# Kernel tuning notes

Hardware: AMD Instinct MI355X
Metric: run time of the kernel (lower is better)

## Reference

```python
import jax, jax.numpy as jnp
import numpy as np

T, B, I, H, O = 512, 128, 512, 512, 12

def setup_inputs() -> dict:
    key = jax.random.key(0)
    ks = jax.random.split(key, 17)
    def w(k, shape):
        # xavier-normal-ish init
        std = float(np.sqrt(2.0 / (shape[0] + shape[-1])))
        return jax.random.normal(k, shape, dtype=jnp.float32) * std
    return {
        "x": jax.random.normal(ks[0], (T, B, I), dtype=jnp.float32),
        "w0": w(ks[1], (O, H)), "wz": w(ks[2], (O, H)), "wr": w(ks[3], (O, H)),
        "ws": w(ks[4], (I, H)),
        "wa": w(ks[5], (H, H)), "ua": w(ks[6], (I, H)), "va": w(ks[7], (H, 1)),
        "u0": w(ks[8], (H, H)), "uz": w(ks[9], (H, H)), "ur": w(ks[10], (H, H)),
        "c0": w(ks[11], (I, H)), "cz": w(ks[12], (I, H)), "cr": w(ks[13], (I, H)),
        "fc_w": w(ks[14], (H, O)),
        "fc_b": jnp.zeros((O,), dtype=jnp.float32),
        "max_labels": 16,
    }

def reference(x, w0, wz, wr, ws, wa, ua, va, u0, uz, ur, c0, cz, cr, fc_w, fc_b, max_labels):
    # x: [T, B, I] encoder states; decode max_labels steps of a Bahdanau-attention GRU.
    s0 = jnp.tanh(x[0] @ ws)              # [B, H]
    out0 = s0 @ fc_w + fc_b               # [B, O]
    U = jnp.einsum('tbi,ih->tbh', x, ua)  # precomputed encoder projection
    va_v = va[:, 0]                       # [H]

    def step(carry, _):
        s, out = carry                                          # [B,H], [B,O]
        e = jnp.einsum('tbh,h->tb', jnp.tanh(s @ wa + U), va_v)  # [T,B] additive scores
        a = jax.nn.softmax(e, axis=0)                           # attention over T
        c = jnp.einsum('tb,tbi->bi', a, x)                      # [B,I] context
        r = jax.nn.sigmoid(out @ wr + s @ ur + c @ cr)
        z = jax.nn.sigmoid(out @ wz + s @ uz + c @ cz)
        sh = jnp.tanh(out @ w0 + (r * s) @ u0 + c @ c0)
        s_new = (1.0 - z) * s + z * sh
        out_new = s_new @ fc_w + fc_b
        return (s_new, out_new), out_new

    _, outs = jax.lax.scan(step, (s0, out0), None, length=max_labels - 1)
    all_outs = jnp.concatenate([out0[None], outs], axis=0)  # [L, B, O]
    return jnp.transpose(all_outs, (1, 0, 2))               # [B, L, O]
```

## Files before the change

kernel.cpp:

```cpp
#include <hip/hip_runtime.h>

#define NSTEP 16

typedef __attribute__((ext_vector_type(8))) short s16x8;
typedef __attribute__((ext_vector_type(4))) float f32x4;
typedef __attribute__((ext_vector_type(2))) float f32x2;

__device__ __forceinline__ float bf2f(unsigned short u){
  union { unsigned int i; float f; } v; v.i = ((unsigned int)u) << 16; return v.f;
}
__device__ __forceinline__ unsigned short f2bf(float f){
  union { float f; unsigned int i; } v; v.f = f;
  unsigned int r = v.i + 0x7fffu + ((v.i >> 16) & 1u);
  return (unsigned short)(r >> 16);
}
__device__ __forceinline__ float fast_rcp(float x){ return __builtin_amdgcn_rcpf(x); }
__device__ __forceinline__ float fast_tanh(float x){
  float e = __expf(2.0f * x);
  return 1.0f - 2.0f * fast_rcp(e + 1.0f);
}
__device__ __forceinline__ float fast_sigmoid(float x){
  return fast_rcp(1.0f + __expf(-x));
}
__device__ __forceinline__ void gload16(const void* g, void* l){
  __builtin_amdgcn_global_load_lds((const __attribute__((address_space(1))) void*)g,
                                   (__attribute__((address_space(3))) void*)l, 16, 0, 0);
}
__device__ __forceinline__ float wave_sum(float v){
#pragma unroll
  for (int off = 32; off; off >>= 1) v += __shfl_xor(v, off, 64);
  return v;
}
__device__ __forceinline__ void fp8x8_dec(uint2 w, float* u){
  f32x2 d0 = __builtin_amdgcn_cvt_pk_f32_fp8(w.x, false);
  f32x2 d1 = __builtin_amdgcn_cvt_pk_f32_fp8(w.x, true);
  f32x2 d2 = __builtin_amdgcn_cvt_pk_f32_fp8(w.y, false);
  f32x2 d3 = __builtin_amdgcn_cvt_pk_f32_fp8(w.y, true);
  u[0] = d0[0]; u[1] = d0[1]; u[2] = d1[0]; u[3] = d1[1];
  u[4] = d2[0]; u[5] = d2[1]; u[6] = d3[0]; u[7] = d3[1];
}
__device__ __forceinline__ s16x8 f32x8_to_bf8(float4 a, float4 b){
  s16x8 t8;
  t8[0] = (short)f2bf(a.x); t8[1] = (short)f2bf(a.y);
  t8[2] = (short)f2bf(a.z); t8[3] = (short)f2bf(a.w);
  t8[4] = (short)f2bf(b.x); t8[5] = (short)f2bf(b.y);
  t8[6] = (short)f2bf(b.z); t8[7] = (short)f2bf(b.w);
  return t8;
}
__device__ __forceinline__ uint2 f32x8_to_fp8(float4 a, float4 b){
  unsigned int lo, hi;
  lo = __builtin_amdgcn_cvt_pk_fp8_f32(a.x, a.y, 0, false);
  lo = __builtin_amdgcn_cvt_pk_fp8_f32(a.z, a.w, lo, true);
  hi = __builtin_amdgcn_cvt_pk_fp8_f32(b.x, b.y, 0, false);
  hi = __builtin_amdgcn_cvt_pk_fp8_f32(b.z, b.w, hi, true);
  uint2 w; w.x = lo; w.y = hi;
  return w;
}
__device__ __forceinline__ unsigned char f2fp8(float f){
  return (unsigned char)(__builtin_amdgcn_cvt_pk_fp8_f32(f, f, 0, false) & 0xff);
}

__global__ __launch_bounds__(256) void castx_k(const float* __restrict__ x,
                                               unsigned char* __restrict__ x8){
  size_t idx = (size_t)blockIdx.x * 256 + threadIdx.x;
  const float* p = x + idx * 8;
  float4 a = *(const float4*)p, b = *(const float4*)(p + 4);
  *(uint2*)(x8 + idx * 8) = f32x8_to_fp8(a, b);
}

struct G8LDS { unsigned char A[128 * 64]; unsigned char B[128 * 64]; };

__global__ __launch_bounds__(512) void ugemm8_k(
    const unsigned char* __restrict__ x8, const unsigned char* __restrict__ Pua8,
    unsigned char* __restrict__ U8){
  __shared__ G8LDS lds;
  const int tid = threadIdx.x;
  const int lane = tid & 63, wid = tid >> 6;
  const int wr = wid >> 2, wc = wid & 3;
  const int mt = blockIdx.y, nt = blockIdx.x;
  f32x4 acc[4][2];
#pragma unroll
  for (int m = 0; m < 4; ++m)
#pragma unroll
    for (int n = 0; n < 2; ++n) acc[m][n] = (f32x4)0.0f;

  const int row = tid >> 2, j = tid & 3;
  const int sc16 = j ^ (row & 3);
  for (int kt = 0; kt < 512; kt += 64){
    __syncthreads();
    gload16(x8  + (size_t)(mt * 128 + row) * 512 + kt + sc16 * 16, &lds.A[tid * 16]);
    gload16(Pua8 + (size_t)(nt * 128 + row) * 512 + kt + sc16 * 16, &lds.B[tid * 16]);
    __syncthreads();
#pragma unroll
    for (int ks = 0; ks < 2; ++ks){
      int g = (lane >> 4) + ks * 4;
      long av[4], bv[2];
#pragma unroll
      for (int m = 0; m < 4; ++m){
        int r = wr * 64 + m * 16 + (lane & 15);
        av[m] = *(const long*)&lds.A[r * 64 + ((g ^ ((r & 3) << 1)) << 3)];
      }
#pragma unroll
      for (int n = 0; n < 2; ++n){
        int c = wc * 32 + n * 16 + (lane & 15);
        bv[n] = *(const long*)&lds.B[c * 64 + ((g ^ ((c & 3) << 1)) << 3)];
      }
#pragma unroll
      for (int m = 0; m < 4; ++m)
#pragma unroll
        for (int n = 0; n < 2; ++n)
          acc[m][n] = __builtin_amdgcn_mfma_f32_16x16x32_fp8_fp8(av[m], bv[n], acc[m][n], 0, 0, 0);
    }
  }
#pragma unroll
  for (int m = 0; m < 4; ++m)
#pragma unroll
    for (int n = 0; n < 2; ++n){
      int r_base = mt * 128 + wr * 64 + m * 16 + ((lane >> 4) << 2);
      int col = nt * 128 + wc * 32 + n * 16 + (lane & 15);
#pragma unroll
      for (int q = 0; q < 4; ++q)
        U8[(size_t)(r_base + q) * 512 + col] = f2fp8(acc[m][n][q] * 0.125f);
    }
}

struct FLDS { unsigned short A[64 * 256]; unsigned short B[64 * 256]; };

template<int EPI, bool AF32>
__device__ __forceinline__ void fgemm_body(int mt, int nt,
    const unsigned short* __restrict__ A, const float* __restrict__ Af,
    const unsigned short* __restrict__ Bt,
    unsigned short* __restrict__ ob0, float* __restrict__ o0,
    const float* __restrict__ e0, const float* __restrict__ e1,
    const float* __restrict__ e2, FLDS& lds){
  const int tid = threadIdx.x;
  const int lane = tid & 63, wid = tid >> 6;
  const int wr = wid >> 1, wc = wid & 1;
  f32x4 acc[2];
  acc[0] = (f32x4)0.0f; acc[1] = (f32x4)0.0f;

  for (int kt = 0; kt < 512; kt += 256){
    if (kt) __syncthreads();
#pragma unroll
    for (int i = 0; i < 4; ++i){
      int s = i * 512 + tid;
      int row = s >> 5, c = s & 31;
      int sc = (c & 24) | ((c & 7) ^ (row & 7));
      if constexpr (AF32){
        const float* ap = Af + (size_t)(mt * 64 + row) * 512 + kt + sc * 8;
        float4 a0 = *(const float4*)ap, a1 = *(const float4*)(ap + 4);
        *(s16x8*)&lds.A[s * 8] = f32x8_to_bf8(a0, a1);
      } else {
        gload16(A + (size_t)(mt * 64 + row) * 512 + kt + sc * 8, &lds.A[s * 8]);
      }
      gload16(Bt + (size_t)(nt * 64 + row) * 512 + kt + sc * 8, &lds.B[s * 8]);
    }
    __syncthreads();
#pragma unroll
    for (int kk = 0; kk < 8; ++kk){
      int kch = kk * 4 + (lane >> 4);
      int ar = wr * 16 + (lane & 15);
      int asw = (kch & 24) | ((kch & 7) ^ (ar & 7));
      s16x8 av = *(const s16x8*)&lds.A[ar * 256 + asw * 8];
#pragma unroll
      for (int n = 0; n < 2; ++n){
        int br = wc * 32 + n * 16 + (lane & 15);
        int bsw = (kch & 24) | ((kch & 7) ^ (br & 7));
        s16x8 bv = *(const s16x8*)&lds.B[br * 256 + bsw * 8];
        acc[n] = __builtin_amdgcn_mfma_f32_16x16x32_bf16(av, bv, acc[n], 0, 0, 0);
      }
    }
  }

#pragma unroll
  for (int n = 0; n < 2; ++n){
    int r_base = mt * 64 + wr * 16 + ((lane >> 4) << 2);
    int col = nt * 64 + wc * 32 + n * 16 + (lane & 15);
#pragma unroll
    for (int q = 0; q < 4; ++q){
      float v = acc[n][q];
      size_t r_ = (size_t)(r_base + q);
      if constexpr (EPI == 1){
        float t = fast_tanh(v);
        o0[r_ * 512 + col] = t;
        ob0[r_ * 512 + col] = f2bf(t);
      } else if constexpr (EPI == 2){
        o0[r_ * 2048 + col] = v + e0[col];
      } else if constexpr (EPI == 4){
        float v2 = v + e0[r_ * 512 + col];
        float sh = fast_tanh(v2);
        float z  = e1[r_ * 512 + col];
        float so = e2[r_ * 512 + col];
        float sn = (1.0f - z) * so + z * sh;
        o0[r_ * 512 + col] = sn;
        ob0[r_ * 512 + col] = f2bf(sn);
      }
    }
  }
}

template<int EPI, bool AF32>
__global__ __launch_bounds__(512) void fgemm_k(
    const unsigned short* __restrict__ A, const float* __restrict__ Af,
    const unsigned short* __restrict__ Bt,
    unsigned short* __restrict__ ob0, float* __restrict__ o0,
    const float* __restrict__ e0, const float* __restrict__ e1,
    const float* __restrict__ e2){
  __shared__ FLDS lds;
  fgemm_body<EPI, AF32>(blockIdx.y, blockIdx.x, A, Af, Bt, ob0, o0, e0, e1, e2, lds);
}

__global__ __launch_bounds__(512) void ec_k(const unsigned char* __restrict__ U8,
    const unsigned char* __restrict__ x8, const float* __restrict__ pre1,
    const float* __restrict__ va, float* __restrict__ cpart, float* __restrict__ psum){
  __shared__ float cred[8][512];
  __shared__ float pred[8];
  int chunk = blockIdx.x, b = blockIdx.y;
  int tid = threadIdx.x, lane = tid & 63, wid = tid >> 6;
  const float* pp = pre1 + (size_t)b * 2048 + lane * 8;
  float4 p0 = *(const float4*)pp, p1 = *(const float4*)(pp + 4);
  const float* vp = va + lane * 8;
  float4 v0 = *(const float4*)vp, v1 = *(const float4*)(vp + 4);
  float sv[8] = {p0.x, p0.y, p0.z, p0.w, p1.x, p1.y, p1.z, p1.w};
  float vv[8] = {v0.x, v0.y, v0.z, v0.w, v1.x, v1.y, v1.z, v1.w};
  float acc[8] = {0, 0, 0, 0, 0, 0, 0, 0};
  float psum_l = 0.f;
  int t0 = chunk * 128 + wid * 16;
  for (int i = 0; i < 16; ++i){
    int t = t0 + i;
    uint2 w = *(const uint2*)(U8 + ((size_t)t * 128 + b) * 512 + lane * 8);
    float u[8];
    fp8x8_dec(w, u);
    float e = 0.f;
#pragma unroll
    for (int k = 0; k < 8; ++k)
      e += fast_tanh(u[k] + sv[k]) * vv[k];
    e = wave_sum(e);
    float p = __expf(e);
    psum_l += p;
    uint2 wx = *(const uint2*)(x8 + ((size_t)t * 128 + b) * 512 + lane * 8);
    float ux[8];
    fp8x8_dec(wx, ux);
#pragma unroll
    for (int k = 0; k < 8; ++k) acc[k] += p * ux[k];
  }
#pragma unroll
  for (int k = 0; k < 8; ++k) cred[wid][lane * 8 + k] = acc[k];
  if (lane == 0) pred[wid] = psum_l;
  __syncthreads();
  float cs = 0.f;
#pragma unroll
  for (int w = 0; w < 8; ++w) cs += cred[w][tid];
  cpart[((size_t)chunk * 128 + b) * 512 + tid] = cs;
  if (tid == 0){
    float s = 0.f;
#pragma unroll
    for (int w = 0; w < 8; ++w) s += pred[w];
    psum[chunk * 128 + b] = s;
  }
}

__global__ __launch_bounds__(512) void gates_k(
    const float* __restrict__ cpart, const float* __restrict__ psum,
    const unsigned short* __restrict__ P2w, const float* __restrict__ pre1,
    const float* __restrict__ s_prev,
    unsigned short* __restrict__ rsb, float* __restrict__ zbuf, float* __restrict__ cu0){
  __shared__ FLDS lds;
  __shared__ float rden_s[64];
  const int tid = threadIdx.x;
  const int lane = tid & 63, wid = tid >> 6;
  const int wr = wid >> 1, wc = wid & 1;
  const int nt = blockIdx.x, mt = blockIdx.y;
  if (tid < 64){
    float d = 0.f;
#pragma unroll
    for (int ch = 0; ch < 4; ++ch) d += psum[ch * 128 + mt * 64 + tid];
    rden_s[tid] = fast_rcp(d);
  }
  f32x4 acc[2];
  acc[0] = (f32x4)0.0f; acc[1] = (f32x4)0.0f;

  for (int kt = 0; kt < 512; kt += 256){
    __syncthreads();
#pragma unroll
    for (int i = 0; i < 4; ++i){
      int s = i * 512 + tid;
      int row = s >> 5, c = s & 31;
      int sc = (c & 24) | ((c & 7) ^ (row & 7));
      int b = mt * 64 + row;
      float rd = rden_s[row];
      float vsum[8] = {0, 0, 0, 0, 0, 0, 0, 0};
#pragma unroll
      for (int ch = 0; ch < 4; ++ch){
        const float* cp = cpart + ((size_t)ch * 128 + b) * 512 + kt + sc * 8;
        float4 a0 = *(const float4*)cp, a1 = *(const float4*)(cp + 4);
        vsum[0] += a0.x; vsum[1] += a0.y; vsum[2] += a0.z; vsum[3] += a0.w;
        vsum[4] += a1.x; vsum[5] += a1.y; vsum[6] += a1.z; vsum[7] += a1.w;
      }
      s16x8 t8;
#pragma unroll
      for (int k = 0; k < 8; ++k) t8[k] = (short)f2bf(vsum[k] * rd);
      *(s16x8*)&lds.A[s * 8] = t8;
      gload16(P2w + (size_t)(nt * 64 + row) * 512 + kt + sc * 8, &lds.B[s * 8]);
    }
    __syncthreads();
#pragma unroll
    for (int kk = 0; kk < 8; ++kk){
      int kch = kk * 4 + (lane >> 4);
      int ar = wr * 16 + (lane & 15);
      int asw = (kch & 24) | ((kch & 7) ^ (ar & 7));
      s16x8 av = *(const s16x8*)&lds.A[ar * 256 + asw * 8];
#pragma unroll
      for (int n = 0; n < 2; ++n){
        int br = wc * 32 + n * 16 + (lane & 15);
        int bsw = (kch & 24) | ((kch & 7) ^ (br & 7));
        s16x8 bv = *(const s16x8*)&lds.B[br * 256 + bsw * 8];
        acc[n] = __builtin_amdgcn_mfma_f32_16x16x32_bf16(av, bv, acc[n], 0, 0, 0);
      }
    }
  }

#pragma unroll
  for (int n = 0; n < 2; ++n){
    int r_base = mt * 64 + wr * 16 + ((lane >> 4) << 2);
    int col = nt * 64 + wc * 32 + n * 16 + (lane & 15);
#pragma unroll
    for (int q = 0; q < 4; ++q){
      float v = acc[n][q];
      size_t r_ = (size_t)(r_base + q);
      float v2 = v + pre1[r_ * 2048 + 512 + col];
      if (col < 512){
        float rg = fast_sigmoid(v2);
        rsb[r_ * 512 + col] = f2bf(rg * s_prev[r_ * 512 + col]);
      } else if (col < 1024){
        zbuf[r_ * 512 + (col - 512)] = fast_sigmoid(v2);
      } else {
        cu0[r_ * 512 + (col - 1024)] = v2;
      }
    }
  }
}

__global__ __launch_bounds__(512) void dout_k(const float* __restrict__ s_hist,
    const float* __restrict__ fcwT, const float* __restrict__ fcb,
    float* __restrict__ dout){
  int lane = threadIdx.x & 63, wid = threadIdx.x >> 6;
  int w = blockIdx.x * 8 + wid;
  int step = w >> 7, b = w & 127;
  const float* sp = s_hist + (size_t)w * 512 + lane * 8;
  float4 sa = *(const float4*)sp, sb = *(const float4*)(sp + 4);
#pragma unroll
  for (int o = 0; o < 12; ++o){
    const float* fp = fcwT + (size_t)o * 512 + lane * 8;
    float4 fa = *(const float4*)fp, fb = *(const float4*)(fp + 4);
    float sum = sa.x * fa.x + sa.y * fa.y + sa.z * fa.z + sa.w * fa.w +
                sb.x * fb.x + sb.y * fb.y + sb.z * fb.z + sb.w * fb.w;
    sum = wave_sum(sum);
    if (lane == 0)
      dout[(size_t)b * (NSTEP * 12) + step * 12 + o] = sum + fcb[o];
  }
}

__global__ __launch_bounds__(512) void trans_k(
    const float* __restrict__ ua, const float* __restrict__ wsm,
    const float* __restrict__ u0, const float* __restrict__ wa,
    const float* __restrict__ urm, const float* __restrict__ uz,
    const float* __restrict__ cr, const float* __restrict__ cz,
    const float* __restrict__ c0, const float* __restrict__ wrm,
    const float* __restrict__ wzm, const float* __restrict__ w0m,
    const float* __restrict__ fcw, const float* __restrict__ fcb,
    unsigned char* __restrict__ Pua8, unsigned short* __restrict__ Pws,
    unsigned short* __restrict__ P3w, unsigned short* __restrict__ P1w,
    unsigned short* __restrict__ P2w, float* __restrict__ fcwT,
    float* __restrict__ bias_full){
  __shared__ unsigned short tr[64][72];
  int bid = blockIdx.x, tid = threadIdx.x;
  if (bid < 640){
    int mi = bid >> 6, tile = bid & 63;
    int trr = tile >> 3, tcc = tile & 7;
    const float* src = nullptr; const float* W = nullptr; unsigned short* dst = nullptr;
    switch (mi){
      case 0: src = ua;  dst = nullptr;           break;
      case 1: src = wsm; dst = Pws;               break;
      case 2: src = u0;  dst = P3w;               break;
      case 3: src = wa;  dst = P1w;               break;
      case 4: src = urm; dst = P1w + 512 * 512;  W = wrm; break;
      case 5: src = uz;  dst = P1w + 1024 * 512; W = wzm; break;
      case 6: src = nullptr; dst = P1w + 1536 * 512; W = w0m; break;
      case 7: src = cr;  dst = P2w;               break;
      case 8: src = cz;  dst = P2w + 512 * 512;   break;
      default:src = c0;  dst = P2w + 1024 * 512;  break;
    }
    int r = tid >> 3, c8 = (tid & 7) * 8;
    int h = trr * 64 + r;
    float vals[8];
    if (src){
      const float* sp = src + (size_t)h * 512 + tcc * 64 + c8;
      float4 a = *(const float4*)sp, b = *(const float4*)(sp + 4);
      vals[0] = a.x; vals[1] = a.y; vals[2] = a.z; vals[3] = a.w;
      vals[4] = b.x; vals[5] = b.y; vals[6] = b.z; vals[7] = b.w;
    } else {
#pragma unroll
      for (int k = 0; k < 8; ++k) vals[k] = 0.f;
    }
    if (W){
      float fr[12];
#pragma unroll
      for (int o = 0; o < 12; ++o) fr[o] = fcw[h * 12 + o];
#pragma unroll
      for (int jj = 0; jj < 8; ++jj){
        int j = tcc * 64 + c8 + jj;
        float cj = 0.f;
#pragma unroll
        for (int o = 0; o < 12; ++o) cj += fr[o] * W[o * 512 + j];
        vals[jj] += cj;
      }
    }
    unsigned short* lp = &tr[r][c8];
#pragma unroll
    for (int k = 0; k < 8; ++k) lp[k] = f2bf(vals[k]);
    __syncthreads();
    if (mi == 0){
      float v[8];
#pragma unroll
      for (int k = 0; k < 8; ++k) v[k] = bf2f(tr[c8 + k][r]) * 8.0f;
      float4 a; a.x = v[0]; a.y = v[1]; a.z = v[2]; a.w = v[3];
      float4 b; b.x = v[4]; b.y = v[5]; b.z = v[6]; b.w = v[7];
      *(uint2*)(Pua8 + (size_t)(tcc * 64 + r) * 512 + trr * 64 + c8) = f32x8_to_fp8(a, b);
    } else {
      s16x8 o8v;
#pragma unroll
      for (int k = 0; k < 8; ++k) o8v[k] = (short)tr[c8 + k][r];
      *(s16x8*)(dst + (size_t)(tcc * 64 + r) * 512 + trr * 64 + c8) = o8v;
    }
  } else if (bid < 652){
    int gidx = (bid - 640) * 512 + tid;
    int h = gidx / 12, o = gidx - h * 12;
    fcwT[(size_t)o * 512 + h] = fcw[h * 12 + o];
  } else {
#pragma unroll
    for (int p = 0; p < 4; ++p){
      int col = p * 512 + tid;
      float v = 0.f;
      if (p > 0){
        const float* W = (p == 1) ? wrm : (p == 2) ? wzm : w0m;
#pragma unroll
        for (int o = 0; o < 12; ++o) v += fcb[o] * W[o * 512 + tid];
      }
      bias_full[col] = v;
    }
  }
}

extern "C" void kernel_launch(void* const* d_in, const int* in_sizes, int n_in,
                              void* d_out, int out_size, void* d_ws, size_t ws_size,
                              hipStream_t stream){
  const float* x   = (const float*)d_in[0];
  const float* w0  = (const float*)d_in[1];
  const float* wz  = (const float*)d_in[2];
  const float* wrm = (const float*)d_in[3];
  const float* wsm = (const float*)d_in[4];
  const float* wa  = (const float*)d_in[5];
  const float* ua  = (const float*)d_in[6];
  const float* va  = (const float*)d_in[7];
  const float* u0  = (const float*)d_in[8];
  const float* uz  = (const float*)d_in[9];
  const float* urm = (const float*)d_in[10];
  const float* c0  = (const float*)d_in[11];
  const float* cz  = (const float*)d_in[12];
  const float* cr  = (const float*)d_in[13];
  const float* fcw = (const float*)d_in[14];
  const float* fcb = (const float*)d_in[15];
  float* dout = (float*)d_out;

  char* base = (char*)d_ws;
  size_t off = 0;
  auto alloc = [&](size_t bytes) -> char* {
    char* p = base + off; off += (bytes + 255) & ~(size_t)255; return p;
  };
  unsigned char*  x8   = (unsigned char*) alloc((size_t)512 * 128 * 512);
  unsigned char*  U8   = (unsigned char*) alloc((size_t)512 * 128 * 512);
  unsigned char*  Pua8 = (unsigned char*) alloc(512 * 512);
  unsigned short* Pws  = (unsigned short*)alloc(512 * 512 * 2);
  unsigned short* P3w  = (unsigned short*)alloc(512 * 512 * 2);
  unsigned short* P1w  = (unsigned short*)alloc((size_t)2048 * 512 * 2);
  unsigned short* P2w  = (unsigned short*)alloc((size_t)1536 * 512 * 2);
  float* fcwT          = (float*)alloc(12 * 512 * 4);
  float* bias_full     = (float*)alloc(2048 * 4);
  float* pre1          = (float*)alloc((size_t)128 * 2048 * 4);
  float* cpart         = (float*)alloc((size_t)4 * 128 * 512 * 4);
  float* psum          = (float*)alloc(4 * 128 * 4);
  unsigned short* rsb  = (unsigned short*)alloc((size_t)128 * 512 * 2);
  float* zbuf          = (float*)alloc((size_t)128 * 512 * 4);
  float* cu0           = (float*)alloc((size_t)128 * 512 * 4);
  float* s_hist        = (float*)alloc((size_t)NSTEP * 128 * 512 * 4);
  unsigned short* s_bf = (unsigned short*)alloc((size_t)128 * 512 * 2);
  (void)ws_size; (void)in_sizes; (void)n_in; (void)out_size;

  trans_k<<<653, 512, 0, stream>>>(ua, wsm, u0, wa, urm, uz, cr, cz, c0,
                                   wrm, wz, w0, fcw, fcb,
                                   Pua8, Pws, P3w, P1w, P2w, fcwT, bias_full);
  castx_k<<<16384, 256, 0, stream>>>(x, x8);
  ugemm8_k<<<dim3(4, 512), 512, 0, stream>>>(x8, Pua8, U8);
  fgemm_k<1, true><<<dim3(8, 2), 512, 0, stream>>>(nullptr, x, Pws, s_bf, s_hist,
                                                   nullptr, nullptr, nullptr);

  for (int step = 1; step < NSTEP; ++step){
    const float* s_prev = s_hist + (size_t)(step - 1) * 128 * 512;
    float* s_cur = s_hist + (size_t)step * 128 * 512;
    fgemm_k<2, false><<<dim3(32, 2), 512, 0, stream>>>(s_bf, nullptr, P1w,
                                                       nullptr, pre1,
                                                       bias_full, nullptr, nullptr);
    ec_k<<<dim3(4, 128), 512, 0, stream>>>(U8, x8, pre1, va, cpart, psum);
    gates_k<<<dim3(24, 2), 512, 0, stream>>>(cpart, psum, P2w, pre1, s_prev,
                                             rsb, zbuf, cu0);
    fgemm_k<4, false><<<dim3(8, 2), 512, 0, stream>>>(rsb, nullptr, P3w,
                                                      s_bf, s_cur,
                                                      cu0, zbuf, s_prev);
  }
  dout_k<<<256, 512, 0, stream>>>(s_hist, fcwT, fcb, dout);
}
```

Measured before the change: 740.3 us.

## Split pre-GEMM and co-schedule its gate part with attention kernel

The per-step GEMM of s against [wa|ur|uz|u0-ish] is split in two. Only the wa projection (512 columns) now runs ahead of the attention kernel. The remaining 1536 columns run inside a fused kernel whose first 48 blocks do that GEMM while the other 512 blocks compute attention scores and context partials. This shortens the critical-path GEMM before attention and overlaps the rest with attention work. In exchange it adds a heterogeneous kernel with a union LDS footprint, which may change occupancy for the attention blocks.

```diff
diff --git a/kernel.cpp b/kernel.cpp
--- a/kernel.cpp
+++ b/kernel.cpp
@@ -184,8 +184,10 @@
         float t = fast_tanh(v);
         o0[r_ * 512 + col] = t;
         ob0[r_ * 512 + col] = f2bf(t);
-      } else if constexpr (EPI == 2){
-        o0[r_ * 2048 + col] = v + e0[col];
+      } else if constexpr (EPI == 5){
+        o0[r_ * 512 + col] = v + e0[col];
+      } else if constexpr (EPI == 6){
+        o0[r_ * 1536 + col] = v + e0[col];
       } else if constexpr (EPI == 4){
         float v2 = v + e0[r_ * 512 + col];
         float sh = fast_tanh(v2);
@@ -210,14 +212,28 @@
   fgemm_body<EPI, AF32>(blockIdx.y, blockIdx.x, A, Af, Bt, ob0, o0, e0, e1, e2, lds);
 }
 
-__global__ __launch_bounds__(512) void ec_k(const unsigned char* __restrict__ U8,
-    const unsigned char* __restrict__ x8, const float* __restrict__ pre1,
-    const float* __restrict__ va, float* __restrict__ cpart, float* __restrict__ psum){
-  __shared__ float cred[8][512];
-  __shared__ float pred[8];
-  int chunk = blockIdx.x, b = blockIdx.y;
+union FusedLDS {
+  FLDS g;
+  struct { float cred[8][512]; float pred[8]; } e;
+};
+
+__global__ __launch_bounds__(512) void fused_k(
+    const unsigned short* __restrict__ s_bf, const unsigned short* __restrict__ P23w,
+    const float* __restrict__ bias23, float* __restrict__ pre23,
+    const unsigned char* __restrict__ U8, const unsigned char* __restrict__ x8,
+    const float* __restrict__ pre_wa, const float* __restrict__ va,
+    float* __restrict__ cpart, float* __restrict__ psum){
+  __shared__ FusedLDS lds;
+  const int bid = blockIdx.x;
+  if (bid < 48){
+    fgemm_body<6, false>(bid & 1, bid >> 1, s_bf, nullptr, P23w,
+                         nullptr, pre23, bias23, nullptr, nullptr, lds.g);
+    return;
+  }
+  const int eb = bid - 48;
+  const int chunk = eb >> 7, b = eb & 127;
   int tid = threadIdx.x, lane = tid & 63, wid = tid >> 6;
-  const float* pp = pre1 + (size_t)b * 2048 + lane * 8;
+  const float* pp = pre_wa + (size_t)b * 512 + lane * 8;
   float4 p0 = *(const float4*)pp, p1 = *(const float4*)(pp + 4);
   const float* vp = va + lane * 8;
   float4 v0 = *(const float4*)vp, v1 = *(const float4*)(vp + 4);
@@ -245,24 +261,24 @@
     for (int k = 0; k < 8; ++k) acc[k] += p * ux[k];
   }
 #pragma unroll
-  for (int k = 0; k < 8; ++k) cred[wid][lane * 8 + k] = acc[k];
-  if (lane == 0) pred[wid] = psum_l;
+  for (int k = 0; k < 8; ++k) lds.e.cred[wid][lane * 8 + k] = acc[k];
+  if (lane == 0) lds.e.pred[wid] = psum_l;
   __syncthreads();
   float cs = 0.f;
 #pragma unroll
-  for (int w = 0; w < 8; ++w) cs += cred[w][tid];
+  for (int w = 0; w < 8; ++w) cs += lds.e.cred[w][tid];
   cpart[((size_t)chunk * 128 + b) * 512 + tid] = cs;
   if (tid == 0){
     float s = 0.f;
 #pragma unroll
-    for (int w = 0; w < 8; ++w) s += pred[w];
+    for (int w = 0; w < 8; ++w) s += lds.e.pred[w];
     psum[chunk * 128 + b] = s;
   }
 }
 
 __global__ __launch_bounds__(512) void gates_k(
     const float* __restrict__ cpart, const float* __restrict__ psum,
-    const unsigned short* __restrict__ P2w, const float* __restrict__ pre1,
+    const unsigned short* __restrict__ P2w, const float* __restrict__ pre23,
     const float* __restrict__ s_prev,
     unsigned short* __restrict__ rsb, float* __restrict__ zbuf, float* __restrict__ cu0){
   __shared__ FLDS lds;
@@ -328,7 +344,7 @@
     for (int q = 0; q < 4; ++q){
       float v = acc[n][q];
       size_t r_ = (size_t)(r_base + q);
-      float v2 = v + pre1[r_ * 2048 + 512 + col];
+      float v2 = v + pre23[r_ * 1536 + col];
       if (col < 512){
         float rg = fast_sigmoid(v2);
         rsb[r_ * 512 + col] = f2bf(rg * s_prev[r_ * 512 + col]);
@@ -487,7 +503,8 @@
   unsigned short* P2w  = (unsigned short*)alloc((size_t)1536 * 512 * 2);
   float* fcwT          = (float*)alloc(12 * 512 * 4);
   float* bias_full     = (float*)alloc(2048 * 4);
-  float* pre1          = (float*)alloc((size_t)128 * 2048 * 4);
+  float* pre_wa        = (float*)alloc((size_t)128 * 512 * 4);
+  float* pre23         = (float*)alloc((size_t)128 * 1536 * 4);
   float* cpart         = (float*)alloc((size_t)4 * 128 * 512 * 4);
   float* psum          = (float*)alloc(4 * 128 * 4);
   unsigned short* rsb  = (unsigned short*)alloc((size_t)128 * 512 * 2);
@@ -508,11 +525,12 @@
   for (int step = 1; step < NSTEP; ++step){
     const float* s_prev = s_hist + (size_t)(step - 1) * 128 * 512;
     float* s_cur = s_hist + (size_t)step * 128 * 512;
-    fgemm_k<2, false><<<dim3(32, 2), 512, 0, stream>>>(s_bf, nullptr, P1w,
-                                                       nullptr, pre1,
-                                                       bias_full, nullptr, nullptr);
-    ec_k<<<dim3(4, 128), 512, 0, stream>>>(U8, x8, pre1, va, cpart, psum);
-    gates_k<<<dim3(24, 2), 512, 0, stream>>>(cpart, psum, P2w, pre1, s_prev,
+    fgemm_k<5, false><<<dim3(8, 2), 512, 0, stream>>>(s_bf, nullptr, P1w,
+                                                      nullptr, pre_wa,
+                                                      bias_full, nullptr, nullptr);
+    fused_k<<<560, 512, 0, stream>>>(s_bf, P1w + 512 * 512, bias_full + 512,
+                                     pre23, U8, x8, pre_wa, va, cpart, psum);
+    gates_k<<<dim3(24, 2), 512, 0, stream>>>(cpart, psum, P2w, pre23, s_prev,
                                              rsb, zbuf, cu0);
     fgemm_k<4, false><<<dim3(8, 2), 512, 0, stream>>>(rsb, nullptr, P3w,
                                                       s_bf, s_cur,
```

New measurement: 842.4 us. 13.8% more time.
